# Optimization experiments

Measured on AMD Instinct MI355X. Metric: run time of the kernel, lower is better.

## Reference

```python
import jax, jax.numpy as jnp
import numpy as np


def setup_inputs() -> dict:
    key = jax.random.key(0)
    ks = jax.random.split(key, 6)
    B, T, D, H = 2, 2048, 1024, 16
    dk = D // H
    s = 0.02
    return {
        "x": jax.random.normal(ks[0], (B, T, D), dtype=jnp.float32),
        "Wq": jax.random.normal(ks[1], (H, dk, dk), dtype=jnp.float32) * s,
        "Wk": jax.random.normal(ks[2], (H, dk, dk), dtype=jnp.float32) * s,
        "Wv": jax.random.normal(ks[3], (H, dk, dk), dtype=jnp.float32) * s,
        "Wp": jax.random.normal(ks[4], (D, D), dtype=jnp.float32) * s,
        "bp": jnp.zeros((D,), dtype=jnp.float32),
    }


def reference(x, Wq, Wk, Wv, Wp, bp):
    B, T, D = x.shape
    H, dk, _ = Wq.shape
    # split into heads: [B, H, T, dk]
    xh = x.reshape(B, T, H, dk).transpose(0, 2, 1, 3)
    # per-head torch Linear (y = x @ W^T), all heads at once
    q = jnp.einsum('bhtd,hkd->bhtk', xh, Wq)
    k = jnp.einsum('bhtd,hkd->bhtk', xh, Wk)
    v = jnp.einsum('bhtd,hkd->bhtk', xh, Wv)
    scale = 1.0 / jnp.sqrt(jnp.float32(dk))  # original divides by sqrt(C) with C == d_k
    scores = jnp.einsum('bhqd,bhkd->bhqk', q, k) * scale
    causal = jnp.tril(jnp.ones((T, T), dtype=bool))
    scores = jnp.where(causal[None, None], scores, -jnp.inf)
    attn = jax.nn.softmax(scores, axis=-1)
    out = jnp.einsum('bhqk,bhkd->bhqd', attn, v)  # [B,H,T,dk]
    out = out.transpose(0, 2, 1, 3).reshape(B, T, D)  # concat heads
    return out @ Wp.T + bp
```

## Files before the change

kernel.cpp:

```cpp
#include <hip/hip_runtime.h>
#include <math.h>

#define B_ 2
#define T_ 2048
#define D_ 1024
#define H_ 16
#define DK 64
#define BH_ (B_*H_)

typedef __attribute__((ext_vector_type(8))) short short8;
typedef __attribute__((ext_vector_type(4))) short bf16x4;
typedef __attribute__((ext_vector_type(4))) float fragC;

#if defined(__HIP_DEVICE_COMPILE__)
#define MFMA16(A,B,C) __builtin_amdgcn_mfma_f32_16x16x16bf16_1k((A),(B),(C),0,0,0)
#else
#define MFMA16(A,B,C) (C)
#endif
#define MFMA32(A,B,C) __builtin_amdgcn_mfma_f32_16x16x32_bf16((A),(B),(C),0,0,0)

__device__ __forceinline__ unsigned short f2bf(float x) {
    union { float f; unsigned u; } c; c.f = x;
    unsigned r = c.u + 0x7fff + ((c.u >> 16) & 1);
    return (unsigned short)(r >> 16);
}

__device__ __forceinline__ unsigned pack2bf(float a, float b) {
    return (unsigned)f2bf(a) | ((unsigned)f2bf(b) << 16);
}

__device__ __forceinline__ unsigned permpack(float a, float b) {
    union { float f; unsigned u; } ca, cb; ca.f = a; cb.f = b;
    return __builtin_amdgcn_perm(cb.u, ca.u, 0x07060302);
}

__device__ __forceinline__ short8 packbf8(float4 a, float4 b) {
    union { short8 v; unsigned u[4]; } r;
    r.u[0] = pack2bf(a.x, a.y); r.u[1] = pack2bf(a.z, a.w);
    r.u[2] = pack2bf(b.x, b.y); r.u[3] = pack2bf(b.z, b.w);
    return r.v;
}

__device__ __forceinline__ void gload_lds16(const void* g, void* l) {
    __builtin_amdgcn_global_load_lds(
        (const __attribute__((address_space(1))) unsigned int*)g,
        (__attribute__((address_space(3))) unsigned int*)l, 16, 0, 0);
}

__global__ __launch_bounds__(256) void cvt_kernel(
    const float* __restrict__ Wp,
    const float* __restrict__ Wq, const float* __restrict__ Wk,
    const float* __restrict__ Wv,
    unsigned short* __restrict__ Wb, unsigned short* __restrict__ wqkvb)
{
    const int gid = blockIdx.x * 256 + threadIdx.x;
    const float* src; unsigned short* dst;
    if (gid < 131072) { src = Wp + (size_t)gid * 8; dst = Wb + (size_t)gid * 8; }
    else              { int e = gid - 131072;
                        int mat = e >> 13, rem = e & 8191;
                        int h = rem >> 9, od = rem & 511;
                        const float* ws = (mat == 0) ? Wq : (mat == 1) ? Wk : Wv;
                        src = ws + ((size_t)(h << 9) + od) * 8;
                        dst = wqkvb + ((size_t)h*1536 + mat*512 + od) * 8; }
    float4 a = *(const float4*)src;
    float4 b = *(const float4*)(src + 4);
    *(uint4*)dst = make_uint4(pack2bf(a.x, a.y), pack2bf(a.z, a.w),
                              pack2bf(b.x, b.y), pack2bf(b.z, b.w));
}

__global__ __launch_bounds__(256) void qkv_kernel(
    const float* __restrict__ x,
    const unsigned short* __restrict__ wqkvb,
    unsigned short* __restrict__ q, unsigned short* __restrict__ k,
    unsigned short* __restrict__ vt)
{
    __shared__ unsigned short Wl[3*64*64];

    const int bh = blockIdx.x;
    const int b  = bh >> 4, h = bh & 15;
    const int t0 = blockIdx.y * 128;
    const int tid = threadIdx.x;
    const int wave = tid >> 6, lane = tid & 63;
    const int n = lane & 15, quad = lane >> 4;

    {
        const unsigned short* wsrc = wqkvb + (size_t)h * 12288;
        #pragma unroll
        for (int j = 0; j < 6; ++j) {
            const int off = (wave*6 + j) * 512 + lane*8;
            gload_lds16(wsrc + off, &Wl[off]);
        }
    }

    const int tw = t0 + wave*32;
    short8 xf[2][2];
    #pragma unroll
    for (int rt = 0; rt < 2; ++rt) {
        const float* xr = &x[((size_t)b*T_ + tw + rt*16 + n)*D_ + h*DK];
        float4 a0 = *(const float4*)&xr[quad*8];
        float4 a1 = *(const float4*)&xr[quad*8 + 4];
        xf[rt][0] = packbf8(a0, a1);
        float4 b0 = *(const float4*)&xr[32 + quad*8];
        float4 b1 = *(const float4*)&xr[32 + quad*8 + 4];
        xf[rt][1] = packbf8(b0, b1);
    }
    __syncthreads();

    const float qsc = 0.125f * 1.44269504088896340736f;
    const int tb0 = blockIdx.y*8 + wave*2;
    #pragma unroll
    for (int mat = 0; mat < 3; ++mat) {
        const int wbase = mat * 4096;
        #pragma unroll
        for (int ct = 0; ct < 4; ++ct) {
            short8 wf0 = *(const short8*)&Wl[wbase + (ct*16 + n)*64 + quad*8];
            short8 wf1 = *(const short8*)&Wl[wbase + (ct*16 + n)*64 + 32 + quad*8];
            if (mat < 2) {
                #pragma unroll
                for (int rt = 0; rt < 2; ++rt) {
                    fragC z = {0.f,0.f,0.f,0.f};
                    z = MFMA32(wf0, xf[rt][0], z);
                    z = MFMA32(wf1, xf[rt][1], z);
                    if (mat == 0) {
                        z[0] *= qsc; z[1] *= qsc; z[2] *= qsc; z[3] *= qsc;
                    }
                    unsigned short* dstg = (mat == 0) ? q : k;
                    unsigned short* dp = &dstg[((size_t)bh*128 + tb0 + rt)*1024
                                               + (ct*2 + (quad>>1))*128 + n*8 + (quad&1)*4];
                    *(uint2*)dp = make_uint2(pack2bf(z[0], z[1]), pack2bf(z[2], z[3]));
                }
            } else {
                uint4 pv4;
                {
                    fragC z = {0.f,0.f,0.f,0.f};
                    z = MFMA32(xf[0][0], wf0, z);
                    z = MFMA32(xf[0][1], wf1, z);
                    pv4.x = pack2bf(z[0], z[1]); pv4.y = pack2bf(z[2], z[3]);
                }
                {
                    fragC z = {0.f,0.f,0.f,0.f};
                    z = MFMA32(xf[1][0], wf0, z);
                    z = MFMA32(xf[1][1], wf1, z);
                    pv4.z = pack2bf(z[0], z[1]); pv4.w = pack2bf(z[2], z[3]);
                }
                const int ktv = tw >> 6, pv = (tw >> 5) & 1;
                unsigned short* dp = &vt[(size_t)bh*131072 + ktv*4096
                                         + ct*1024 + pv*512 + lane*8];
                *(uint4*)dp = pv4;
            }
        }
    }
}

__global__ __launch_bounds__(256, 2) void attn_kernel(
    const unsigned short* __restrict__ q, const unsigned short* __restrict__ k,
    const unsigned short* __restrict__ vt, unsigned short* __restrict__ aout)
{
    __shared__ fragC Os[4][4][4][64];
    __shared__ float Ls[4][4][16];

    const int id = blockIdx.x;
    const int x  = id & 7, p = id >> 3;
    const int jj = p & 3, s = p >> 2, g = s & 7, r = s >> 3;
    const int bh = x*4 + jj;
    const int qt = (r == 0) ? 31 - g : (r == 1) ? g : (r == 2) ? 23 - g : 8 + g;

    const int b   = bh >> 4, h = bh & 15;
    const int tid = threadIdx.x;
    const int w = tid >> 6, lane = tid & 63;
    const int n = lane & 15, quad = lane >> 4;

    short8 qf[4][2];
    #pragma unroll
    for (int qc = 0; qc < 4; ++qc) {
        const unsigned short* qb = &q[((size_t)bh*128 + qt*4 + qc)*1024 + n*8];
        qf[qc][0] = *(const short8*)&qb[quad*128];
        qf[qc][1] = *(const short8*)&qb[(4 + quad)*128];
    }

    fragC o[4][4];
    #pragma unroll
    for (int qc = 0; qc < 4; ++qc)
        #pragma unroll
        for (int dt = 0; dt < 4; ++dt) o[qc][dt] = (fragC){0.f,0.f,0.f,0.f};
    fragC l[4];
    #pragma unroll
    for (int qc = 0; qc < 4; ++qc) l[qc] = (fragC){0.f,0.f,0.f,0.f};

    bf16x4 ones4;
    #pragma unroll
    for (int jo = 0; jo < 4; ++jo) ones4[jo] = (short)0x3F80;

    const unsigned short* kg = &k[(size_t)bh*131072 + lane*8];
    const unsigned short* vg = &vt[(size_t)bh*131072 + lane*8];
    const int nt = qt + 1;

    short8 kf[4][2];
    short8 vv[4][2];

    int t = w;
    if (t < nt) {
        #pragma unroll
        for (int ct = 0; ct < 4; ++ct) {
            kf[ct][0] = *(const short8*)&kg[t*4096 + ct*1024];
            kf[ct][1] = *(const short8*)&kg[t*4096 + ct*1024 + 512];
        }
    }

    for (; t < nt; t += 4) {
        #pragma unroll
        for (int dt = 0; dt < 4; ++dt) {
            vv[dt][0] = *(const short8*)&vg[t*4096 + dt*1024];
            vv[dt][1] = *(const short8*)&vg[t*4096 + dt*1024 + 512];
        }

        const bool diag = (t == qt);
        #pragma unroll
        for (int qp = 0; qp < 2; ++qp) {
            bf16x4 pp[2][4];
            #pragma unroll
            for (int q2 = 0; q2 < 2; ++q2) {
                const int qc = qp*2 + q2;
                #pragma unroll
                for (int ct = 0; ct < 4; ++ct) {
                    fragC c = (fragC){0.f,0.f,0.f,0.f};
                    c = MFMA32(kf[ct][0], qf[qc][0], c);
                    c = MFMA32(kf[ct][1], qf[qc][1], c);
                    float p0 = exp2f(c[0]), p1 = exp2f(c[1]);
                    float p2 = exp2f(c[2]), p3 = exp2f(c[3]);
                    if (diag) {
                        const int lim = (qc*16 + n) - (ct*16 + quad*4);
                        if (0 > lim) p0 = 0.f;
                        if (1 > lim) p1 = 0.f;
                        if (2 > lim) p2 = 0.f;
                        if (3 > lim) p3 = 0.f;
                    }
                    union { bf16x4 v; unsigned u[2]; } pk;
                    pk.u[0] = permpack(p0, p1);
                    pk.u[1] = permpack(p2, p3);
                    pp[q2][ct] = pk.v;
                }
            }

            if (qp == 1 && t + 4 < nt) {
                #pragma unroll
                for (int ct = 0; ct < 4; ++ct) {
                    kf[ct][0] = *(const short8*)&kg[(t+4)*4096 + ct*1024];
                    kf[ct][1] = *(const short8*)&kg[(t+4)*4096 + ct*1024 + 512];
                }
            }

            #pragma unroll
            for (int q2 = 0; q2 < 2; ++q2) {
                const int qc = qp*2 + q2;
                #pragma unroll
                for (int ct = 0; ct < 4; ++ct)
                    l[qc] = MFMA16(ones4, pp[q2][ct], l[qc]);
            }

            #pragma unroll
            for (int q2 = 0; q2 < 2; ++q2) {
                const int qc = qp*2 + q2;
                #pragma unroll
                for (int dt = 0; dt < 4; ++dt) {
                    #pragma unroll
                    for (int ct = 0; ct < 4; ++ct) {
                        union { short8 s8; bf16x4 hh[2]; } uv;
                        uv.s8 = vv[dt][ct >> 1];
                        o[qc][dt] = MFMA16(uv.hh[ct & 1], pp[q2][ct], o[qc][dt]);
                    }
                }
            }
        }
    }

    #pragma unroll
    for (int qc = 0; qc < 4; ++qc) {
        #pragma unroll
        for (int dt = 0; dt < 4; ++dt)
            Os[w][qc][dt][lane] = o[qc][dt];
        if (quad == 0) Ls[w][qc][n] = l[qc][0];
    }
    __syncthreads();

    const float lsum = Ls[0][w][n] + Ls[1][w][n] + Ls[2][w][n] + Ls[3][w][n];
    const float inv = 1.0f / lsum;
    const int q0 = qt*64 + w*16;
    unsigned short* dp = &aout[((size_t)b*T_ + q0 + n)*D_ + h*DK + quad*4];
    #pragma unroll
    for (int dt = 0; dt < 4; ++dt) {
        fragC sum = Os[0][w][dt][lane] + Os[1][w][dt][lane]
                  + Os[2][w][dt][lane] + Os[3][w][dt][lane];
        *(uint2*)(dp + dt*16) =
            make_uint2(pack2bf(sum[0]*inv, sum[1]*inv),
                       pack2bf(sum[2]*inv, sum[3]*inv));
    }
}

__global__ __launch_bounds__(256) void proj_kernel(
    const unsigned short* __restrict__ A, const unsigned short* __restrict__ Wb,
    const float* __restrict__ bp, float* __restrict__ out)
{
    __shared__ unsigned short As[128*64];
    __shared__ unsigned short Bs[128*64];

    const int m0 = blockIdx.x * 128, n0 = blockIdx.y * 128;
    const int tid = threadIdx.x;
    const int wave = tid >> 6, lane = tid & 63;
    const int wm = wave & 1, wn = wave >> 1;
    const int n = lane & 15, quad = lane >> 4;

    const int srow = wave*32 + (lane >> 3);
    const int scol = (lane & 7) * 8;
    const unsigned short* ag = &A [(size_t)(m0 + srow)*1024 + scol];
    const unsigned short* bg = &Wb[(size_t)(n0 + srow)*1024 + scol];
    unsigned short* al = &As[(size_t)srow*64 + scol];
    unsigned short* bl = &Bs[(size_t)srow*64 + scol];

    fragC acc[4][4];
    #pragma unroll
    for (int i = 0; i < 4; ++i)
        #pragma unroll
        for (int j = 0; j < 4; ++j) acc[i][j] = (fragC){0.f,0.f,0.f,0.f};

    for (int kt = 0; kt < 16; ++kt) {
        __syncthreads();
        #pragma unroll
        for (int i = 0; i < 4; ++i) {
            gload_lds16(ag + (size_t)i*8*1024 + kt*64, al + i*8*64);
            gload_lds16(bg + (size_t)i*8*1024 + kt*64, bl + i*8*64);
        }
        __syncthreads();

        #pragma unroll
        for (int kk = 0; kk < 2; ++kk) {
            short8 af[4], bf[4];
            #pragma unroll
            for (int i = 0; i < 4; ++i)
                af[i] = *(const short8*)&As[(wm*64 + i*16 + n)*64 + kk*32 + quad*8];
            #pragma unroll
            for (int j = 0; j < 4; ++j)
                bf[j] = *(const short8*)&Bs[(wn*64 + j*16 + n)*64 + kk*32 + quad*8];
            #pragma unroll
            for (int i = 0; i < 4; ++i)
                #pragma unroll
                for (int j = 0; j < 4; ++j)
                    acc[i][j] = MFMA32(af[i], bf[j], acc[i][j]);
        }
    }

    #pragma unroll
    for (int i = 0; i < 4; ++i) {
        #pragma unroll
        for (int r = 0; r < 4; ++r) {
            const int m = m0 + wm*64 + i*16 + quad*4 + r;
            #pragma unroll
            for (int j = 0; j < 4; ++j) {
                const int col = n0 + wn*64 + j*16 + n;
                out[(size_t)m*1024 + col] = acc[i][j][r] + bp[col];
            }
        }
    }
}

extern "C" void kernel_launch(void* const* d_in, const int* in_sizes, int n_in,
                              void* d_out, int out_size, void* d_ws, size_t ws_size,
                              hipStream_t stream)
{
    const float* x  = (const float*)d_in[0];
    const float* Wq = (const float*)d_in[1];
    const float* Wk = (const float*)d_in[2];
    const float* Wv = (const float*)d_in[3];
    const float* Wp = (const float*)d_in[4];
    const float* bp = (const float*)d_in[5];
    float* out = (float*)d_out;

    const size_t per = (size_t)BH_ * T_ * DK;
    unsigned short* qws   = (unsigned short*)d_ws;
    unsigned short* kws   = qws + per;
    unsigned short* vtws  = kws + per;
    unsigned short* aws   = vtws + per;
    unsigned short* wbws  = aws + per;
    unsigned short* wqkvb = wbws + 1024*1024;

    cvt_kernel<<<dim3(608), 256, 0, stream>>>(Wp, Wq, Wk, Wv, wbws, wqkvb);
    qkv_kernel<<<dim3(BH_, T_/128), 256, 0, stream>>>(x, wqkvb, qws, kws, vtws);
    attn_kernel<<<dim3(1024), 256, 0, stream>>>(qws, kws, vtws, aws);
    proj_kernel<<<dim3(32, 8), 256, 0, stream>>>(aws, wbws, bp, out);
}
```

Baseline: 141.6 us.

## Fold weight conversion into qkv, use 32-wide MFMA for PV, double-buffer proj

Removes the separate weight-conversion kernel. The qkv kernel now converts Wp to bf16 for the projection and converts its own head's Wq/Wk/Wv directly into LDS, which saves one launch and a round trip of the converted weights. The attention inner loop switches the P·V and row-sum products from 16x16x16 to 16x16x32 bf16 MFMA, packing eight probabilities per operand, and brackets the MFMA sections with s_setprio. The projection GEMM gets double-buffered LDS staging with a single barrier per k-step and a remapped 1D grid for better tile locality, at the cost of twice the LDS.

```diff
diff --git a/kernel.cpp b/kernel.cpp
--- a/kernel.cpp
+++ b/kernel.cpp
@@ -9,14 +9,8 @@
 #define BH_ (B_*H_)
 
 typedef __attribute__((ext_vector_type(8))) short short8;
-typedef __attribute__((ext_vector_type(4))) short bf16x4;
 typedef __attribute__((ext_vector_type(4))) float fragC;
 
-#if defined(__HIP_DEVICE_COMPILE__)
-#define MFMA16(A,B,C) __builtin_amdgcn_mfma_f32_16x16x16bf16_1k((A),(B),(C),0,0,0)
-#else
-#define MFMA16(A,B,C) (C)
-#endif
 #define MFMA32(A,B,C) __builtin_amdgcn_mfma_f32_16x16x32_bf16((A),(B),(C),0,0,0)
 
 __device__ __forceinline__ unsigned short f2bf(float x) {
@@ -47,30 +41,11 @@
         (__attribute__((address_space(3))) unsigned int*)l, 16, 0, 0);
 }
 
-__global__ __launch_bounds__(256) void cvt_kernel(
-    const float* __restrict__ Wp,
-    const float* __restrict__ Wq, const float* __restrict__ Wk,
-    const float* __restrict__ Wv,
-    unsigned short* __restrict__ Wb, unsigned short* __restrict__ wqkvb)
-{
-    const int gid = blockIdx.x * 256 + threadIdx.x;
-    const float* src; unsigned short* dst;
-    if (gid < 131072) { src = Wp + (size_t)gid * 8; dst = Wb + (size_t)gid * 8; }
-    else              { int e = gid - 131072;
-                        int mat = e >> 13, rem = e & 8191;
-                        int h = rem >> 9, od = rem & 511;
-                        const float* ws = (mat == 0) ? Wq : (mat == 1) ? Wk : Wv;
-                        src = ws + ((size_t)(h << 9) + od) * 8;
-                        dst = wqkvb + ((size_t)h*1536 + mat*512 + od) * 8; }
-    float4 a = *(const float4*)src;
-    float4 b = *(const float4*)(src + 4);
-    *(uint4*)dst = make_uint4(pack2bf(a.x, a.y), pack2bf(a.z, a.w),
-                              pack2bf(b.x, b.y), pack2bf(b.z, b.w));
-}
-
 __global__ __launch_bounds__(256) void qkv_kernel(
     const float* __restrict__ x,
-    const unsigned short* __restrict__ wqkvb,
+    const float* __restrict__ Wq, const float* __restrict__ Wk,
+    const float* __restrict__ Wv, const float* __restrict__ Wp,
+    unsigned short* __restrict__ Wb,
     unsigned short* __restrict__ q, unsigned short* __restrict__ k,
     unsigned short* __restrict__ vt)
 {
@@ -84,11 +59,27 @@
     const int n = lane & 15, quad = lane >> 4;
 
     {
-        const unsigned short* wsrc = wqkvb + (size_t)h * 12288;
-        #pragma unroll
-        for (int j = 0; j < 6; ++j) {
-            const int off = (wave*6 + j) * 512 + lane*8;
-            gload_lds16(wsrc + off, &Wl[off]);
+        const int L = bh + (blockIdx.y << 5);
+        const float* src = Wp + (size_t)L*2048 + tid*8;
+        float4 a = *(const float4*)src;
+        float4 b2 = *(const float4*)(src + 4);
+        *(uint4*)(Wb + (size_t)L*2048 + tid*8) =
+            make_uint4(pack2bf(a.x, a.y), pack2bf(a.z, a.w),
+                       pack2bf(b2.x, b2.y), pack2bf(b2.z, b2.w));
+    }
+
+    #pragma unroll
+    for (int mat = 0; mat < 3; ++mat) {
+        const float* ws = ((mat == 0) ? Wq : (mat == 1) ? Wk : Wv)
+                          + (size_t)h * 4096;
+        #pragma unroll
+        for (int j = 0; j < 2; ++j) {
+            const int e = (j*256 + tid) * 8;
+            float4 a = *(const float4*)&ws[e];
+            float4 b2 = *(const float4*)&ws[e + 4];
+            *(uint4*)&Wl[mat*4096 + e] =
+                make_uint4(pack2bf(a.x, a.y), pack2bf(a.z, a.w),
+                           pack2bf(b2.x, b2.y), pack2bf(b2.z, b2.w));
         }
     }
 
@@ -160,9 +151,9 @@
     __shared__ float Ls[4][4][16];
 
     const int id = blockIdx.x;
-    const int x  = id & 7, p = id >> 3;
+    const int xc = id & 7, p = id >> 3;
     const int jj = p & 3, s = p >> 2, g = s & 7, r = s >> 3;
-    const int bh = x*4 + jj;
+    const int bh = xc*4 + jj;
     const int qt = (r == 0) ? 31 - g : (r == 1) ? g : (r == 2) ? 23 - g : 8 + g;
 
     const int b   = bh >> 4, h = bh & 15;
@@ -187,9 +178,9 @@
     #pragma unroll
     for (int qc = 0; qc < 4; ++qc) l[qc] = (fragC){0.f,0.f,0.f,0.f};
 
-    bf16x4 ones4;
-    #pragma unroll
-    for (int jo = 0; jo < 4; ++jo) ones4[jo] = (short)0x3F80;
+    short8 ones8;
+    #pragma unroll
+    for (int jo = 0; jo < 8; ++jo) ones8[jo] = (short)0x3F80;
 
     const unsigned short* kg = &k[(size_t)bh*131072 + lane*8];
     const unsigned short* vg = &vt[(size_t)bh*131072 + lane*8];
@@ -216,18 +207,26 @@
 
         const bool diag = (t == qt);
         #pragma unroll
-        for (int qp = 0; qp < 2; ++qp) {
-            bf16x4 pp[2][4];
-            #pragma unroll
-            for (int q2 = 0; q2 < 2; ++q2) {
-                const int qc = qp*2 + q2;
-                #pragma unroll
-                for (int ct = 0; ct < 4; ++ct) {
-                    fragC c = (fragC){0.f,0.f,0.f,0.f};
-                    c = MFMA32(kf[ct][0], qf[qc][0], c);
-                    c = MFMA32(kf[ct][1], qf[qc][1], c);
-                    float p0 = exp2f(c[0]), p1 = exp2f(c[1]);
-                    float p2 = exp2f(c[2]), p3 = exp2f(c[3]);
+        for (int qc = 0; qc < 4; ++qc) {
+            union { short8 v; unsigned u[4]; } pb[2];
+            #pragma unroll
+            for (int cp = 0; cp < 2; ++cp) {
+                fragC c[2];
+                __builtin_amdgcn_s_setprio(1);
+                #pragma unroll
+                for (int c2 = 0; c2 < 2; ++c2) {
+                    const int ct = cp*2 + c2;
+                    fragC z = {0.f,0.f,0.f,0.f};
+                    z = MFMA32(kf[ct][0], qf[qc][0], z);
+                    z = MFMA32(kf[ct][1], qf[qc][1], z);
+                    c[c2] = z;
+                }
+                __builtin_amdgcn_s_setprio(0);
+                #pragma unroll
+                for (int c2 = 0; c2 < 2; ++c2) {
+                    const int ct = cp*2 + c2;
+                    float p0 = exp2f(c[c2][0]), p1 = exp2f(c[c2][1]);
+                    float p2 = exp2f(c[c2][2]), p3 = exp2f(c[c2][3]);
                     if (diag) {
                         const int lim = (qc*16 + n) - (ct*16 + quad*4);
                         if (0 > lim) p0 = 0.f;
@@ -235,14 +234,12 @@
                         if (2 > lim) p2 = 0.f;
                         if (3 > lim) p3 = 0.f;
                     }
-                    union { bf16x4 v; unsigned u[2]; } pk;
-                    pk.u[0] = permpack(p0, p1);
-                    pk.u[1] = permpack(p2, p3);
-                    pp[q2][ct] = pk.v;
-                }
-            }
-
-            if (qp == 1 && t + 4 < nt) {
+                    pb[cp].u[c2*2]     = permpack(p0, p1);
+                    pb[cp].u[c2*2 + 1] = permpack(p2, p3);
+                }
+            }
+
+            if (qc == 3 && t + 4 < nt) {
                 #pragma unroll
                 for (int ct = 0; ct < 4; ++ct) {
                     kf[ct][0] = *(const short8*)&kg[(t+4)*4096 + ct*1024];
@@ -250,27 +247,15 @@
                 }
             }
 
-            #pragma unroll
-            for (int q2 = 0; q2 < 2; ++q2) {
-                const int qc = qp*2 + q2;
-                #pragma unroll
-                for (int ct = 0; ct < 4; ++ct)
-                    l[qc] = MFMA16(ones4, pp[q2][ct], l[qc]);
-            }
-
-            #pragma unroll
-            for (int q2 = 0; q2 < 2; ++q2) {
-                const int qc = qp*2 + q2;
-                #pragma unroll
-                for (int dt = 0; dt < 4; ++dt) {
-                    #pragma unroll
-                    for (int ct = 0; ct < 4; ++ct) {
-                        union { short8 s8; bf16x4 hh[2]; } uv;
-                        uv.s8 = vv[dt][ct >> 1];
-                        o[qc][dt] = MFMA16(uv.hh[ct & 1], pp[q2][ct], o[qc][dt]);
-                    }
-                }
-            }
+            __builtin_amdgcn_s_setprio(1);
+            #pragma unroll
+            for (int pv = 0; pv < 2; ++pv) {
+                l[qc] = MFMA32(ones8, pb[pv].v, l[qc]);
+                #pragma unroll
+                for (int dt = 0; dt < 4; ++dt)
+                    o[qc][dt] = MFMA32(vv[dt][pv], pb[pv].v, o[qc][dt]);
+            }
+            __builtin_amdgcn_s_setprio(0);
         }
     }
 
@@ -301,10 +286,12 @@
     const unsigned short* __restrict__ A, const unsigned short* __restrict__ Wb,
     const float* __restrict__ bp, float* __restrict__ out)
 {
-    __shared__ unsigned short As[128*64];
-    __shared__ unsigned short Bs[128*64];
-
-    const int m0 = blockIdx.x * 128, n0 = blockIdx.y * 128;
+    __shared__ unsigned short As[2][128*64];
+    __shared__ unsigned short Bs[2][128*64];
+
+    const int id = blockIdx.x;
+    const int m0 = (((id & 7) << 2) + ((id >> 3) >> 3)) << 7;
+    const int n0 = (((id >> 3) & 7)) << 7;
     const int tid = threadIdx.x;
     const int wave = tid >> 6, lane = tid & 63;
     const int wm = wave & 1, wn = wave >> 1;
@@ -314,8 +301,6 @@
     const int scol = (lane & 7) * 8;
     const unsigned short* ag = &A [(size_t)(m0 + srow)*1024 + scol];
     const unsigned short* bg = &Wb[(size_t)(n0 + srow)*1024 + scol];
-    unsigned short* al = &As[(size_t)srow*64 + scol];
-    unsigned short* bl = &Bs[(size_t)srow*64 + scol];
 
     fragC acc[4][4];
     #pragma unroll
@@ -323,24 +308,31 @@
         #pragma unroll
         for (int j = 0; j < 4; ++j) acc[i][j] = (fragC){0.f,0.f,0.f,0.f};
 
+    auto stage = [&](int bu, int kt) {
+        unsigned short* al = &As[bu][srow*64 + scol];
+        unsigned short* bl = &Bs[bu][srow*64 + scol];
+        #pragma unroll
+        for (int i = 0; i < 4; ++i) {
+            gload_lds16(ag + (size_t)i*8192 + kt*64, al + i*512);
+            gload_lds16(bg + (size_t)i*8192 + kt*64, bl + i*512);
+        }
+    };
+
+    stage(0, 0);
     for (int kt = 0; kt < 16; ++kt) {
         __syncthreads();
-        #pragma unroll
-        for (int i = 0; i < 4; ++i) {
-            gload_lds16(ag + (size_t)i*8*1024 + kt*64, al + i*8*64);
-            gload_lds16(bg + (size_t)i*8*1024 + kt*64, bl + i*8*64);
-        }
-        __syncthreads();
-
+        if (kt < 15) stage((kt + 1) & 1, kt + 1);
+        const unsigned short* Ab = As[kt & 1];
+        const unsigned short* Bb = Bs[kt & 1];
         #pragma unroll
         for (int kk = 0; kk < 2; ++kk) {
             short8 af[4], bf[4];
             #pragma unroll
             for (int i = 0; i < 4; ++i)
-                af[i] = *(const short8*)&As[(wm*64 + i*16 + n)*64 + kk*32 + quad*8];
+                af[i] = *(const short8*)&Ab[(wm*64 + i*16 + n)*64 + kk*32 + quad*8];
             #pragma unroll
             for (int j = 0; j < 4; ++j)
-                bf[j] = *(const short8*)&Bs[(wn*64 + j*16 + n)*64 + kk*32 + quad*8];
+                bf[j] = *(const short8*)&Bb[(wn*64 + j*16 + n)*64 + kk*32 + quad*8];
             #pragma unroll
             for (int i = 0; i < 4; ++i)
                 #pragma unroll
@@ -381,10 +373,9 @@
     unsigned short* vtws  = kws + per;
     unsigned short* aws   = vtws + per;
     unsigned short* wbws  = aws + per;
-    unsigned short* wqkvb = wbws + 1024*1024;
-
-    cvt_kernel<<<dim3(608), 256, 0, stream>>>(Wp, Wq, Wk, Wv, wbws, wqkvb);
-    qkv_kernel<<<dim3(BH_, T_/128), 256, 0, stream>>>(x, wqkvb, qws, kws, vtws);
+
+    qkv_kernel<<<dim3(BH_, T_/128), 256, 0, stream>>>(x, Wq, Wk, Wv, Wp, wbws,
+                                                      qws, kws, vtws);
     attn_kernel<<<dim3(1024), 256, 0, stream>>>(qws, kws, vtws, aws);
-    proj_kernel<<<dim3(32, 8), 256, 0, stream>>>(aws, wbws, bp, out);
-}
+    proj_kernel<<<dim3(256), 256, 0, stream>>>(aws, wbws, bp, out);
+}
```

Result: no change. 139.3 us (-1.6%).
